# Optimization experiments

Measured on AMD Instinct MI355X. Metric: run time of the kernel, lower is better.

## Reference

```python
import jax, jax.numpy as jnp
import numpy as np

NT, NH, NW = 16, 16, 16
HEADS, DIM_HEAD = 8, 64
DIM = 512
DEPTH = 4
EPS = 1e-5


def _layernorm(x, g, b):
    mu = jnp.mean(x, axis=-1, keepdims=True)
    var = jnp.mean(jnp.square(x - mu), axis=-1, keepdims=True)
    return (x - mu) * jax.lax.rsqrt(var + EPS) * g + b


def setup_inputs() -> dict:
    key = jax.random.key(0)
    ks = jax.random.split(key, 4)
    n = NT * NH * NW
    inner = HEADS * DIM_HEAD
    x = jax.random.normal(ks[0], (8, n, DIM), dtype=jnp.float32)
    Wqkv = jax.random.normal(ks[1], (DEPTH, DIM, 3 * inner), dtype=jnp.float32) * (DIM ** -0.5)
    Wout = jax.random.normal(ks[2], (DEPTH, inner, DIM), dtype=jnp.float32) * (inner ** -0.5)
    bout = jnp.zeros((DEPTH, DIM), dtype=jnp.float32)
    gamma = jnp.ones((DEPTH, DIM), dtype=jnp.float32)
    beta = jnp.zeros((DEPTH, DIM), dtype=jnp.float32)
    return {"x": x, "Wqkv": Wqkv, "Wout": Wout, "bout": bout, "gamma": gamma, "beta": beta}


def _fda_layer(x, Wqkv, Wout, bout, g, bb):
    b, n, d = x.shape
    hs = HEADS // 2
    s = NH * NW
    scale = DIM_HEAD ** -0.5
    y = _layernorm(x, g, bb)
    qkv = y @ Wqkv  # (b, n, 3*inner)
    q, k, v = jnp.split(qkv, 3, axis=-1)
    # b n (h d) -> b h n d
    def to_heads(t):
        return t.reshape(b, n, HEADS, DIM_HEAD).transpose(0, 2, 1, 3)
    q, k, v = to_heads(q), to_heads(k), to_heads(v)
    # spatial branch: first half of heads, view n as (t, s)
    qs = q[:, :hs].reshape(b, hs, NT, s, DIM_HEAD)
    ks = k[:, :hs].reshape(b, hs, NT, s, DIM_HEAD)
    vs = v[:, :hs].reshape(b, hs, NT, s, DIM_HEAD)
    sp_dots = jnp.einsum('bhtid,bhtjd->bhtij', qs, ks) * scale
    sp_attn = jax.nn.softmax(sp_dots, axis=-1)
    sp_out = jnp.einsum('bhtij,bhtjd->bhtid', sp_attn, vs)  # (b,hs,nt,s,dh)
    # temporal branch: second half of heads, view n as (s, t)
    qt = q[:, hs:].reshape(b, hs, s, NT, DIM_HEAD)
    kt = k[:, hs:].reshape(b, hs, s, NT, DIM_HEAD)
    vt = v[:, hs:].reshape(b, hs, s, NT, DIM_HEAD)
    tp_dots = jnp.einsum('bhsid,bhsjd->bhsij', qt, kt) * scale
    tp_attn = jax.nn.softmax(tp_dots, axis=-1)
    tp_out = jnp.einsum('bhsij,bhsjd->bhsid', tp_attn, vt)  # (b,hs,s,nt,dh)
    out = jnp.concatenate([sp_out.reshape(b, hs, n, DIM_HEAD),
                           tp_out.reshape(b, hs, n, DIM_HEAD)], axis=1)  # (b,h,n,dh)
    out = out.transpose(0, 2, 1, 3).reshape(b, n, HEADS * DIM_HEAD)
    return out @ Wout + bout


def reference(x, Wqkv, Wout, bout, gamma, beta):
    for l in range(DEPTH):
        x = _fda_layer(x, Wqkv[l], Wout[l], bout[l], gamma[l], beta[l]) + x
    return x
```

## Files before the change

kernel.cpp:

```cpp
#include <hip/hip_runtime.h>
#include <hip/hip_bf16.h>

typedef __bf16 bf16x8 __attribute__((ext_vector_type(8)));
typedef float f32x4 __attribute__((ext_vector_type(4)));

#define AS1(p) ((const __attribute__((address_space(1))) void*)(p))
#define AS3(p) ((__attribute__((address_space(3))) void*)(p))

__global__ __launch_bounds__(256) void cast_transpose(const float* __restrict__ W,
                                                      __bf16* __restrict__ WT,
                                                      int K, int N, int total) {
  int idx = blockIdx.x * 256 + threadIdx.x;
  if (idx >= total) return;
  int nk = N * K;
  int lyr = idx / nk;
  int r = idx - lyr * nk;
  int n = r / K;
  int k = r - n * K;
  WT[idx] = (__bf16)W[(size_t)lyr * nk + (size_t)k * N + n];
}

__global__ __launch_bounds__(256) void ln_kernel(const float* __restrict__ x,
                                                 const float* __restrict__ gamma,
                                                 const float* __restrict__ beta,
                                                 __bf16* __restrict__ y) {
  int wave = threadIdx.x >> 6, lane = threadIdx.x & 63;
  size_t row = (size_t)blockIdx.x * 4 + wave;
  const float* xr = x + row * 512 + lane * 8;
  float4 v0 = *(const float4*)xr;
  float4 v1 = *(const float4*)(xr + 4);
  float s = v0.x + v0.y + v0.z + v0.w + v1.x + v1.y + v1.z + v1.w;
  float ss = v0.x * v0.x + v0.y * v0.y + v0.z * v0.z + v0.w * v0.w +
             v1.x * v1.x + v1.y * v1.y + v1.z * v1.z + v1.w * v1.w;
#pragma unroll
  for (int m = 1; m < 64; m <<= 1) {
    s += __shfl_xor(s, m);
    ss += __shfl_xor(ss, m);
  }
  float mean = s * (1.f / 512.f);
  float var = ss * (1.f / 512.f) - mean * mean;
  float rstd = rsqrtf(var + 1e-5f);
  const float* gp = gamma + lane * 8;
  const float* bp = beta + lane * 8;
  float4 g0 = *(const float4*)gp, g1 = *(const float4*)(gp + 4);
  float4 b0 = *(const float4*)bp, b1 = *(const float4*)(bp + 4);
  bf16x8 o;
  o[0] = (__bf16)((v0.x - mean) * rstd * g0.x + b0.x);
  o[1] = (__bf16)((v0.y - mean) * rstd * g0.y + b0.y);
  o[2] = (__bf16)((v0.z - mean) * rstd * g0.z + b0.z);
  o[3] = (__bf16)((v0.w - mean) * rstd * g0.w + b0.w);
  o[4] = (__bf16)((v1.x - mean) * rstd * g1.x + b1.x);
  o[5] = (__bf16)((v1.y - mean) * rstd * g1.y + b1.y);
  o[6] = (__bf16)((v1.z - mean) * rstd * g1.z + b1.z);
  o[7] = (__bf16)((v1.w - mean) * rstd * g1.w + b1.w);
  *(bf16x8*)(y + row * 512 + lane * 8) = o;
}


#define STAGE_PART(kt_, part_)                                                   \
  {                                                                              \
    const __bf16* gb_ = ((part_) < 2) ? Abase : Bbase;                           \
    int rowoff_ = ((part_)&1) * 128;                                             \
    const __bf16* g0_ = gb_ + (size_t)(rowoff_ + r0s) * 512 + (kt_)*64 + s0 * 8; \
    const __bf16* g1_ = gb_ + (size_t)(rowoff_ + r1s) * 512 + (kt_)*64 + s1 * 8; \
    char* lb_ = lds + (((kt_)&1) * 65536) + ((part_)*16384);                     \
    __builtin_amdgcn_global_load_lds(AS1(g0_), AS3(lb_ + ldsw0), 16, 0, 0);      \
    __builtin_amdgcn_global_load_lds(AS1(g1_), AS3(lb_ + ldsw1), 16, 0, 0);      \
  }

template <int NCOLS, int MODE>
__global__ __launch_bounds__(512, 2) void gemm256(const __bf16* __restrict__ A,
                                                  const __bf16* __restrict__ BT,
                                                  __bf16* __restrict__ Cb,
                                                  float* Cf,
                                                  const float* __restrict__ bias,
                                                  const float* Resid) {
  extern __shared__ __attribute__((aligned(128))) char lds[];
  constexpr int NT = NCOLS / 256;
  int bid = blockIdx.x;
  int cpx = gridDim.x >> 3;
  int L = (bid & 7) * cpx + (bid >> 3);
  int tileM = L / NT, tileN = L - tileM * NT;
  int tid = threadIdx.x;
  int l = tid & 63, w = tid >> 6;
  int lm = l & 15, lh = l >> 4;
  int wave_m = w >> 2, wave_n = w & 3;
  const __bf16* Abase = A + (size_t)tileM * 256 * 512;
  const __bf16* Bbase = BT + (size_t)tileN * 256 * 512;
  int r0s = tid >> 3, s0 = (tid & 7) ^ (r0s & 7);
  int p1 = tid + 512;
  int r1s = p1 >> 3, s1 = (p1 & 7) ^ (r1s & 7);
  int ldsw0 = (w * 64) * 16, ldsw1 = (512 + w * 64) * 16;

  f32x4 acc[8][4];
#pragma unroll
  for (int m = 0; m < 8; ++m)
#pragma unroll
    for (int n = 0; n < 4; ++n) acc[m][n] = (f32x4){0.f, 0.f, 0.f, 0.f};

  int xorv = (lm & 7) << 4;
  int kb0 = (lh * 16) ^ xorv;
  int kb1 = (64 + lh * 16) ^ xorv;
  int arow = wave_m * 128 + lm;
  int brow = wave_n * 64 + lm;

  STAGE_PART(0, 0); STAGE_PART(0, 1); STAGE_PART(0, 2); STAGE_PART(0, 3);

  for (int kt = 0; kt < 8; ++kt) {
    char* sb = lds + (kt & 1) * 65536;
    if (kt < 7) {
      STAGE_PART(kt + 1, 0);
      asm volatile("s_waitcnt vmcnt(2)" ::: "memory");
    } else {
      asm volatile("s_waitcnt vmcnt(0)" ::: "memory");
    }
    __builtin_amdgcn_sched_barrier(0);
    __builtin_amdgcn_s_barrier();
    bf16x8 bfrag[4][2];
#pragma unroll
    for (int nf = 0; nf < 4; ++nf) {
      const char* bp = sb + 32768 + (brow + nf * 16) * 128;
      bfrag[nf][0] = *(const bf16x8*)(bp + kb0);
      bfrag[nf][1] = *(const bf16x8*)(bp + kb1);
    }
#pragma unroll
    for (int ph = 0; ph < 4; ++ph) {
      bf16x8 af[2][2];
#pragma unroll
      for (int m = 0; m < 2; ++m) {
        const char* ap = sb + (arow + (ph * 2 + m) * 16) * 128;
        af[m][0] = *(const bf16x8*)(ap + kb0);
        af[m][1] = *(const bf16x8*)(ap + kb1);
      }
      if (ph == 1 && kt < 7) STAGE_PART(kt + 1, 1);
      if (ph == 2 && kt < 7) STAGE_PART(kt + 1, 2);
      if (ph == 3 && kt < 7) STAGE_PART(kt + 1, 3);
      __builtin_amdgcn_s_barrier();
      __builtin_amdgcn_s_setprio(1);
#pragma unroll
      for (int m = 0; m < 2; ++m)
#pragma unroll
        for (int nf = 0; nf < 4; ++nf) {
          acc[ph * 2 + m][nf] = __builtin_amdgcn_mfma_f32_16x16x32_bf16(
              af[m][0], bfrag[nf][0], acc[ph * 2 + m][nf], 0, 0, 0);
          acc[ph * 2 + m][nf] = __builtin_amdgcn_mfma_f32_16x16x32_bf16(
              af[m][1], bfrag[nf][1], acc[ph * 2 + m][nf], 0, 0, 0);
        }
      __builtin_amdgcn_s_setprio(0);
    }
    __builtin_amdgcn_s_barrier();
  }

  int crow = tileM * 256 + wave_m * 128 + lh * 4;
  int ccol = tileN * 256 + wave_n * 64 + lm;
#pragma unroll
  for (int mf = 0; mf < 8; ++mf)
#pragma unroll
    for (int nf = 0; nf < 4; ++nf) {
      int col = ccol + nf * 16;
#pragma unroll
      for (int r = 0; r < 4; ++r) {
        size_t idx = (size_t)(crow + mf * 16 + r) * NCOLS + col;
        if (MODE == 0) {
          Cb[idx] = (__bf16)acc[mf][nf][r];
        } else {
          Cf[idx] = acc[mf][nf][r] + bias[col] + Resid[idx];
        }
      }
    }
}

__global__ __launch_bounds__(256) void attn_spatial(const __bf16* __restrict__ qkv,
                                                    __bf16* __restrict__ attn_out) {
  __shared__ __attribute__((aligned(16))) __bf16 VT[64 * 256];
  __shared__ __attribute__((aligned(16))) __bf16 P[4][4096];
  int bid = blockIdx.x;
  int b = bid >> 6;
  int rem = bid & 63;
  int h = rem >> 4;
  int t = rem & 15;
  int tid = threadIdx.x;
  int w = tid >> 6, l = tid & 63;
  size_t nbase = (size_t)b * 4096 + t * 256;
#pragma unroll
  for (int i = 0; i < 8; i++) {
    int idx = tid + i * 256;
    int key = idx >> 3, dseg = idx & 7;
    bf16x8 v = *(const bf16x8*)(qkv + (nbase + key) * 1536 + 1024 + h * 64 + dseg * 8);
#pragma unroll
    for (int d2 = 0; d2 < 8; d2++) {
      int dh = dseg * 8 + d2;
      VT[dh * 256 + (((key >> 3) ^ (dh & 7)) << 3) + (key & 7)] = v[d2];
    }
  }
  __syncthreads();
  int lm = l & 15, lh = l >> 4;
  for (int it = 0; it < 4; ++it) {
    int qbase = it * 64 + w * 16;
    const __bf16* qp = qkv + (nbase + qbase + lm) * 1536 + h * 64 + lh * 8;
    bf16x8 aq0 = *(const bf16x8*)qp;
    bf16x8 aq1 = *(const bf16x8*)(qp + 32);
    f32x4 sa[16];
#pragma unroll
    for (int tn = 0; tn < 16; ++tn) {
      const __bf16* kp = qkv + (nbase + tn * 16 + lm) * 1536 + 512 + h * 64 + lh * 8;
      bf16x8 bk0 = *(const bf16x8*)kp;
      bf16x8 bk1 = *(const bf16x8*)(kp + 32);
      f32x4 z = {0.f, 0.f, 0.f, 0.f};
      z = __builtin_amdgcn_mfma_f32_16x16x32_bf16(aq0, bk0, z, 0, 0, 0);
      sa[tn] = __builtin_amdgcn_mfma_f32_16x16x32_bf16(aq1, bk1, z, 0, 0, 0);
    }
    float rmax[4] = {-1e30f, -1e30f, -1e30f, -1e30f};
#pragma unroll
    for (int tn = 0; tn < 16; ++tn)
#pragma unroll
      for (int r = 0; r < 4; ++r) {
        sa[tn][r] *= 0.125f;
        rmax[r] = fmaxf(rmax[r], sa[tn][r]);
      }
#pragma unroll
    for (int m = 1; m < 16; m <<= 1)
#pragma unroll
      for (int r = 0; r < 4; ++r) rmax[r] = fmaxf(rmax[r], __shfl_xor(rmax[r], m));
    float rsum[4] = {0.f, 0.f, 0.f, 0.f};
#pragma unroll
    for (int tn = 0; tn < 16; ++tn)
#pragma unroll
      for (int r = 0; r < 4; ++r) {
        float e = __expf(sa[tn][r] - rmax[r]);
        sa[tn][r] = e;
        rsum[r] += e;
      }
#pragma unroll
    for (int m = 1; m < 16; m <<= 1)
#pragma unroll
      for (int r = 0; r < 4; ++r) rsum[r] += __shfl_xor(rsum[r], m);
    float rinv[4];
#pragma unroll
    for (int r = 0; r < 4; ++r) rinv[r] = 1.f / rsum[r];
#pragma unroll
    for (int tn = 0; tn < 16; ++tn)
#pragma unroll
      for (int r = 0; r < 4; ++r) {
        int row = lh * 4 + r;
        int col = tn * 16 + lm;
        P[w][row * 256 + ((((col >> 3)) ^ (row & 7)) << 3) + (col & 7)] =
            (__bf16)(sa[tn][r] * rinv[r]);
      }
    f32x4 oa[4];
#pragma unroll
    for (int nt = 0; nt < 4; ++nt) oa[nt] = (f32x4){0.f, 0.f, 0.f, 0.f};
#pragma unroll
    for (int kc = 0; kc < 8; ++kc) {
      bf16x8 pa = *(const bf16x8*)&P[w][lm * 256 + (((kc * 4 + lh) ^ (lm & 7)) << 3)];
#pragma unroll
      for (int nt = 0; nt < 4; ++nt) {
        int dh = nt * 16 + lm;
        bf16x8 bv = *(const bf16x8*)&VT[dh * 256 + (((kc * 4 + lh) ^ (dh & 7)) << 3)];
        oa[nt] = __builtin_amdgcn_mfma_f32_16x16x32_bf16(pa, bv, oa[nt], 0, 0, 0);
      }
    }
#pragma unroll
    for (int nt = 0; nt < 4; ++nt)
#pragma unroll
      for (int r = 0; r < 4; ++r) {
        size_t row = nbase + qbase + lh * 4 + r;
        attn_out[row * 512 + h * 64 + nt * 16 + lm] = (__bf16)oa[nt][r];
      }
  }
}

__global__ __launch_bounds__(256) void attn_temporal(const __bf16* __restrict__ qkv,
                                                     __bf16* __restrict__ attn_out) {
  __shared__ __attribute__((aligned(16))) __bf16 VT[4][64 * 40];
  __shared__ __attribute__((aligned(16))) __bf16 P[4][16 * 40];
  int tid = threadIdx.x;
  {
    float4 z4 = {0.f, 0.f, 0.f, 0.f};
#pragma unroll
    for (int i = 0; i < 5; ++i) ((float4*)&VT[0][0])[tid + i * 256] = z4;
    if (tid < 64) ((float4*)&P[0][0])[tid + 256] = z4;
    ((float4*)&P[0][0])[tid] = z4;
  }
  __syncthreads();
  int bid = blockIdx.x;
  int b = bid >> 8;
  int rem = bid & 255;
  int h = 4 + (rem >> 6);
  int g = rem & 63;
  int w = tid >> 6, l = tid & 63;
  int lm = l & 15, lh = l >> 4;
  int sid = g * 4 + w;
  size_t n0 = (size_t)b * 4096 + sid * 16;

  const __bf16* qp = qkv + (n0 + lm) * 1536 + h * 64 + lh * 8;
  bf16x8 aq0 = *(const bf16x8*)qp;
  bf16x8 aq1 = *(const bf16x8*)(qp + 32);
  const __bf16* kp = qp + 512;
  bf16x8 bk0 = *(const bf16x8*)kp;
  bf16x8 bk1 = *(const bf16x8*)(kp + 32);
  int kk = l >> 2;
  int dh0 = (l & 3) * 8;
  const __bf16* vp = qkv + (n0 + kk) * 1536 + 1024 + h * 64 + dh0;
  bf16x8 vr0 = *(const bf16x8*)vp;
  bf16x8 vr1 = *(const bf16x8*)(vp + 32);

  f32x4 s4 = {0.f, 0.f, 0.f, 0.f};
  s4 = __builtin_amdgcn_mfma_f32_16x16x32_bf16(aq0, bk0, s4, 0, 0, 0);
  s4 = __builtin_amdgcn_mfma_f32_16x16x32_bf16(aq1, bk1, s4, 0, 0, 0);

#pragma unroll
  for (int d2 = 0; d2 < 8; ++d2) VT[w][(dh0 + d2) * 40 + kk] = vr0[d2];
#pragma unroll
  for (int d2 = 0; d2 < 8; ++d2) VT[w][(dh0 + 32 + d2) * 40 + kk] = vr1[d2];

  float e[4], rm = -1e30f, rs = 0.f;
#pragma unroll
  for (int r = 0; r < 4; ++r) {
    e[r] = s4[r] * 0.125f;
    rm = fmaxf(rm, e[r]);
  }
  float rmax[4];
#pragma unroll
  for (int r = 0; r < 4; ++r) rmax[r] = e[r];
#pragma unroll
  for (int m = 1; m < 16; m <<= 1)
#pragma unroll
    for (int r = 0; r < 4; ++r) rmax[r] = fmaxf(rmax[r], __shfl_xor(rmax[r], m));
  float rsum[4];
#pragma unroll
  for (int r = 0; r < 4; ++r) {
    e[r] = __expf(e[r] - rmax[r]);
    rsum[r] = e[r];
  }
#pragma unroll
  for (int m = 1; m < 16; m <<= 1)
#pragma unroll
    for (int r = 0; r < 4; ++r) rsum[r] += __shfl_xor(rsum[r], m);
#pragma unroll
  for (int r = 0; r < 4; ++r)
    P[w][(lh * 4 + r) * 40 + lm] = (__bf16)(e[r] / rsum[r]);

  asm volatile("s_waitcnt lgkmcnt(0)" ::: "memory");
  __builtin_amdgcn_sched_barrier(0);

  bf16x8 pa = *(const bf16x8*)&P[w][lm * 40 + lh * 8];
#pragma unroll
  for (int nt = 0; nt < 4; ++nt) {
    bf16x8 bv = *(const bf16x8*)&VT[w][(nt * 16 + lm) * 40 + lh * 8];
    f32x4 oa = {0.f, 0.f, 0.f, 0.f};
    oa = __builtin_amdgcn_mfma_f32_16x16x32_bf16(pa, bv, oa, 0, 0, 0);
#pragma unroll
    for (int r = 0; r < 4; ++r)
      attn_out[(n0 + lh * 4 + r) * 512 + h * 64 + nt * 16 + lm] = (__bf16)oa[r];
  }
}

extern "C" void kernel_launch(void* const* d_in, const int* in_sizes, int n_in,
                              void* d_out, int out_size, void* d_ws, size_t ws_size,
                              hipStream_t stream) {
  const float* x = (const float*)d_in[0];
  const float* Wqkv = (const float*)d_in[1];
  const float* Wout = (const float*)d_in[2];
  const float* bout = (const float*)d_in[3];
  const float* gamma = (const float*)d_in[4];
  const float* beta = (const float*)d_in[5];
  float* out = (float*)d_out;

  const size_t OFF_WOUT = 6291456;
  const size_t OFF_Y = OFF_WOUT + 2097152;
  const size_t OFF_QKV = OFF_Y + 33554432;
  const size_t NEEDED = OFF_QKV + 100663296;
  if (ws_size < NEEDED) return;
  char* ws = (char*)d_ws;
  __bf16* WqkvT = (__bf16*)ws;
  __bf16* WoutT = (__bf16*)(ws + OFF_WOUT);
  __bf16* ybuf = (__bf16*)(ws + OFF_Y);
  __bf16* qkv = (__bf16*)(ws + OFF_QKV);

  hipFuncSetAttribute((const void*)gemm256<1536, 0>,
                      hipFuncAttributeMaxDynamicSharedMemorySize, 131072);
  hipFuncSetAttribute((const void*)gemm256<512, 1>,
                      hipFuncAttributeMaxDynamicSharedMemorySize, 131072);

  cast_transpose<<<12288, 256, 0, stream>>>(Wqkv, WqkvT, 512, 1536, 4 * 512 * 1536);
  cast_transpose<<<4096, 256, 0, stream>>>(Wout, WoutT, 512, 512, 4 * 512 * 512);

  for (int layer = 0; layer < 4; ++layer) {
    const float* src = (layer == 0) ? x : out;
    ln_kernel<<<8192, 256, 0, stream>>>(src, gamma + layer * 512, beta + layer * 512, ybuf);
    gemm256<1536, 0><<<768, 512, 131072, stream>>>(
        ybuf, WqkvT + (size_t)layer * 1536 * 512, qkv, nullptr, nullptr, nullptr);
    attn_spatial<<<512, 256, 0, stream>>>(qkv, ybuf);
    attn_temporal<<<2048, 256, 0, stream>>>(qkv, ybuf);
    gemm256<512, 1><<<256, 512, 131072, stream>>>(
        ybuf, WoutT + (size_t)layer * 512 * 512, nullptr, out, bout + layer * 512, src);
  }
}
```

Before: 766.0 us.

## Use 128x128 tiled out-projection GEMM with LDS-staged coalesced residual epilogue

```diff
diff --git a/kernel.cpp b/kernel.cpp
--- a/kernel.cpp
+++ b/kernel.cpp
@@ -7,17 +7,20 @@
 #define AS1(p) ((const __attribute__((address_space(1))) void*)(p))
 #define AS3(p) ((__attribute__((address_space(3))) void*)(p))
 
-__global__ __launch_bounds__(256) void cast_transpose(const float* __restrict__ W,
-                                                      __bf16* __restrict__ WT,
-                                                      int K, int N, int total) {
-  int idx = blockIdx.x * 256 + threadIdx.x;
-  if (idx >= total) return;
-  int nk = N * K;
-  int lyr = idx / nk;
-  int r = idx - lyr * nk;
-  int n = r / K;
-  int k = r - n * K;
-  WT[idx] = (__bf16)W[(size_t)lyr * nk + (size_t)k * N + n];
+__global__ __launch_bounds__(256) void transpose32(const float* __restrict__ W,
+                                                   __bf16* __restrict__ WT,
+                                                   int K, int N) {
+  __shared__ float t[32][33];
+  int l = blockIdx.z;
+  int k0 = blockIdx.y * 32, n0 = blockIdx.x * 32;
+  int tx = threadIdx.x & 31, ty = threadIdx.x >> 5;
+  const float* src = W + ((size_t)l * K + k0) * N + n0;
+#pragma unroll
+  for (int i = 0; i < 32; i += 8) t[ty + i][tx] = src[(size_t)(ty + i) * N + tx];
+  __syncthreads();
+  __bf16* dst = WT + ((size_t)l * N + n0) * K + k0;
+#pragma unroll
+  for (int i = 0; i < 32; i += 8) dst[(size_t)(ty + i) * K + tx] = (__bf16)t[tx][ty + i];
 }
 
 __global__ __launch_bounds__(256) void ln_kernel(const float* __restrict__ x,
@@ -56,7 +59,6 @@
   *(bf16x8*)(y + row * 512 + lane * 8) = o;
 }
 
-
 #define STAGE_PART(kt_, part_)                                                   \
   {                                                                              \
     const __bf16* gb_ = ((part_) < 2) ? Abase : Bbase;                           \
@@ -68,13 +70,10 @@
     __builtin_amdgcn_global_load_lds(AS1(g1_), AS3(lb_ + ldsw1), 16, 0, 0);      \
   }
 
-template <int NCOLS, int MODE>
+template <int NCOLS>
 __global__ __launch_bounds__(512, 2) void gemm256(const __bf16* __restrict__ A,
                                                   const __bf16* __restrict__ BT,
-                                                  __bf16* __restrict__ Cb,
-                                                  float* Cf,
-                                                  const float* __restrict__ bias,
-                                                  const float* Resid) {
+                                                  __bf16* __restrict__ Cb) {
   extern __shared__ __attribute__((aligned(128))) char lds[];
   constexpr int NT = NCOLS / 256;
   int bid = blockIdx.x;
@@ -161,13 +160,133 @@
 #pragma unroll
       for (int r = 0; r < 4; ++r) {
         size_t idx = (size_t)(crow + mf * 16 + r) * NCOLS + col;
-        if (MODE == 0) {
-          Cb[idx] = (__bf16)acc[mf][nf][r];
-        } else {
-          Cf[idx] = acc[mf][nf][r] + bias[col] + Resid[idx];
-        }
-      }
-    }
+        Cb[idx] = (__bf16)acc[mf][nf][r];
+      }
+    }
+}
+
+#define STAGE_PART128(kt_, part_)                                               \
+  {                                                                             \
+    const __bf16* gb_ = ((part_) < 2) ? Abase : Bbase;                          \
+    int rowoff_ = ((part_)&1) * 64;                                             \
+    const __bf16* g0_ = gb_ + (size_t)(rowoff_ + r0s) * 512 + (kt_)*64 + s0 * 8;\
+    const __bf16* g1_ = gb_ + (size_t)(rowoff_ + r1s) * 512 + (kt_)*64 + s1 * 8;\
+    char* lb_ = lds + (((kt_)&1) * 32768) + (((part_) < 2) ? 0 : 16384) +       \
+                ((part_)&1) * 8192;                                             \
+    __builtin_amdgcn_global_load_lds(AS1(g0_), AS3(lb_ + ldsw0), 16, 0, 0);     \
+    __builtin_amdgcn_global_load_lds(AS1(g1_), AS3(lb_ + ldsw1), 16, 0, 0);     \
+  }
+
+__global__ __launch_bounds__(256, 2) void gemm128res(const __bf16* __restrict__ A,
+                                                     const __bf16* __restrict__ BT,
+                                                     float* Cf,
+                                                     const float* __restrict__ bias,
+                                                     const float* Resid) {
+  extern __shared__ __attribute__((aligned(128))) char lds[];
+  constexpr int NCOLS = 512;
+  constexpr int NT = 4;
+  int bid = blockIdx.x;
+  int cpx = gridDim.x >> 3;
+  int L = (bid & 7) * cpx + (bid >> 3);
+  int tileM = L / NT, tileN = L - tileM * NT;
+  int tid = threadIdx.x;
+  int l = tid & 63, w = tid >> 6;
+  int lm = l & 15, lh = l >> 4;
+  int wave_m = w >> 1, wave_n = w & 1;
+  const __bf16* Abase = A + (size_t)tileM * 128 * 512;
+  const __bf16* Bbase = BT + (size_t)tileN * 128 * 512;
+  int r0s = tid >> 3, s0 = (tid & 7) ^ (r0s & 7);
+  int p1 = tid + 256;
+  int r1s = p1 >> 3, s1 = (p1 & 7) ^ (r1s & 7);
+  int ldsw0 = (w * 64) * 16, ldsw1 = (256 + w * 64) * 16;
+
+  f32x4 acc[4][4];
+#pragma unroll
+  for (int m = 0; m < 4; ++m)
+#pragma unroll
+    for (int n = 0; n < 4; ++n) acc[m][n] = (f32x4){0.f, 0.f, 0.f, 0.f};
+
+  int xorv = (lm & 7) << 4;
+  int kb0 = (lh * 16) ^ xorv;
+  int kb1 = (64 + lh * 16) ^ xorv;
+  int arow = wave_m * 64 + lm;
+  int brow = wave_n * 64 + lm;
+
+  STAGE_PART128(0, 0); STAGE_PART128(0, 1); STAGE_PART128(0, 2); STAGE_PART128(0, 3);
+
+  for (int kt = 0; kt < 8; ++kt) {
+    char* sb = lds + (kt & 1) * 32768;
+    if (kt < 7) {
+      STAGE_PART128(kt + 1, 0);
+      asm volatile("s_waitcnt vmcnt(2)" ::: "memory");
+    } else {
+      asm volatile("s_waitcnt vmcnt(0)" ::: "memory");
+    }
+    __builtin_amdgcn_sched_barrier(0);
+    __builtin_amdgcn_s_barrier();
+    bf16x8 bfrag[4][2];
+#pragma unroll
+    for (int nf = 0; nf < 4; ++nf) {
+      const char* bp = sb + 16384 + (brow + nf * 16) * 128;
+      bfrag[nf][0] = *(const bf16x8*)(bp + kb0);
+      bfrag[nf][1] = *(const bf16x8*)(bp + kb1);
+    }
+#pragma unroll
+    for (int ph = 0; ph < 4; ++ph) {
+      bf16x8 af0, af1;
+      {
+        const char* ap = sb + (arow + ph * 16) * 128;
+        af0 = *(const bf16x8*)(ap + kb0);
+        af1 = *(const bf16x8*)(ap + kb1);
+      }
+      if (ph == 1 && kt < 7) STAGE_PART128(kt + 1, 1);
+      if (ph == 2 && kt < 7) STAGE_PART128(kt + 1, 2);
+      if (ph == 3 && kt < 7) STAGE_PART128(kt + 1, 3);
+      __builtin_amdgcn_s_barrier();
+      __builtin_amdgcn_s_setprio(1);
+#pragma unroll
+      for (int nf = 0; nf < 4; ++nf) {
+        acc[ph][nf] = __builtin_amdgcn_mfma_f32_16x16x32_bf16(af0, bfrag[nf][0],
+                                                              acc[ph][nf], 0, 0, 0);
+        acc[ph][nf] = __builtin_amdgcn_mfma_f32_16x16x32_bf16(af1, bfrag[nf][1],
+                                                              acc[ph][nf], 0, 0, 0);
+      }
+      __builtin_amdgcn_s_setprio(0);
+    }
+    __builtin_amdgcn_s_barrier();
+  }
+
+  float* lf = (float*)(lds + w * 8192);
+  int crow0 = tileM * 128 + wave_m * 64;
+  int ccol0 = tileN * 128 + wave_n * 64;
+  int erow = l >> 2;
+  int ecl = (l & 3) * 4;
+  float4 b4[4];
+#pragma unroll
+  for (int j = 0; j < 4; ++j)
+    b4[j] = *(const float4*)(bias + ccol0 + ecl + j * 16);
+#pragma unroll
+  for (int mf = 0; mf < 4; ++mf) {
+#pragma unroll
+    for (int nf = 0; nf < 4; ++nf)
+#pragma unroll
+      for (int r = 0; r < 4; ++r)
+        lf[(lh * 4 + r) * 68 + nf * 16 + lm] = acc[mf][nf][r];
+    size_t rowg = (size_t)(crow0 + mf * 16 + erow);
+    const float* rp = Resid + rowg * NCOLS + ccol0 + ecl;
+    float* cp = Cf + rowg * NCOLS + ccol0 + ecl;
+#pragma unroll
+    for (int j = 0; j < 4; ++j) {
+      float4 a4 = *(float4*)&lf[erow * 68 + ecl + j * 16];
+      float4 r4 = *(const float4*)(rp + j * 16);
+      float4 o4;
+      o4.x = a4.x + b4[j].x + r4.x;
+      o4.y = a4.y + b4[j].y + r4.y;
+      o4.z = a4.z + b4[j].z + r4.z;
+      o4.w = a4.w + b4[j].w + r4.w;
+      *(float4*)(cp + j * 16) = o4;
+    }
+  }
 }
 
 __global__ __launch_bounds__(256) void attn_spatial(const __bf16* __restrict__ qkv,
@@ -314,15 +433,13 @@
 #pragma unroll
   for (int d2 = 0; d2 < 8; ++d2) VT[w][(dh0 + 32 + d2) * 40 + kk] = vr1[d2];
 
-  float e[4], rm = -1e30f, rs = 0.f;
+  float e[4];
+  float rmax[4];
 #pragma unroll
   for (int r = 0; r < 4; ++r) {
     e[r] = s4[r] * 0.125f;
-    rm = fmaxf(rm, e[r]);
-  }
-  float rmax[4];
-#pragma unroll
-  for (int r = 0; r < 4; ++r) rmax[r] = e[r];
+    rmax[r] = e[r];
+  }
 #pragma unroll
   for (int m = 1; m < 16; m <<= 1)
 #pragma unroll
@@ -378,22 +495,22 @@
   __bf16* ybuf = (__bf16*)(ws + OFF_Y);
   __bf16* qkv = (__bf16*)(ws + OFF_QKV);
 
-  hipFuncSetAttribute((const void*)gemm256<1536, 0>,
+  hipFuncSetAttribute((const void*)gemm256<1536>,
                       hipFuncAttributeMaxDynamicSharedMemorySize, 131072);
-  hipFuncSetAttribute((const void*)gemm256<512, 1>,
-                      hipFuncAttributeMaxDynamicSharedMemorySize, 131072);
-
-  cast_transpose<<<12288, 256, 0, stream>>>(Wqkv, WqkvT, 512, 1536, 4 * 512 * 1536);
-  cast_transpose<<<4096, 256, 0, stream>>>(Wout, WoutT, 512, 512, 4 * 512 * 512);
+  hipFuncSetAttribute((const void*)gemm128res,
+                      hipFuncAttributeMaxDynamicSharedMemorySize, 65536);
+
+  transpose32<<<dim3(48, 16, 4), 256, 0, stream>>>(Wqkv, WqkvT, 512, 1536);
+  transpose32<<<dim3(16, 16, 4), 256, 0, stream>>>(Wout, WoutT, 512, 512);
 
   for (int layer = 0; layer < 4; ++layer) {
     const float* src = (layer == 0) ? x : out;
     ln_kernel<<<8192, 256, 0, stream>>>(src, gamma + layer * 512, beta + layer * 512, ybuf);
-    gemm256<1536, 0><<<768, 512, 131072, stream>>>(
-        ybuf, WqkvT + (size_t)layer * 1536 * 512, qkv, nullptr, nullptr, nullptr);
+    gemm256<1536><<<768, 512, 131072, stream>>>(
+        ybuf, WqkvT + (size_t)layer * 1536 * 512, qkv);
     attn_spatial<<<512, 256, 0, stream>>>(qkv, ybuf);
     attn_temporal<<<2048, 256, 0, stream>>>(qkv, ybuf);
-    gemm256<512, 1><<<256, 512, 131072, stream>>>(
-        ybuf, WoutT + (size_t)layer * 512 * 512, nullptr, out, bout + layer * 512, src);
-  }
-}
+    gemm128res<<<1024, 256, 65536, stream>>>(
+        ybuf, WoutT + (size_t)layer * 512 * 512, out, bout + layer * 512, src);
+  }
+}
```

Result: faster. 667.5 us (-12.9%).
